# Performance work log

Measured on AMD Instinct MI355X. Metric: run time of the kernel, lower is better.

## Reference

```python
import jax, jax.numpy as jnp
import numpy as np

B, V, L, C = 4, 8, 256, 1024
H, O = 16, 4
Dh = C // H
NEG = -1e9

def setup_inputs() -> dict:
    key = jax.random.key(0)
    ks = jax.random.split(key, 16)
    inp = {}
    inp['v'] = jax.random.normal(ks[0], (B, V, L, C), jnp.float32)
    inp['k'] = jax.random.normal(ks[1], (B, V, L, C), jnp.float32)
    inp['q'] = jax.random.normal(ks[2], (B, V, L, C), jnp.float32)
    inp['masks'] = jax.random.uniform(ks[3], (O, B, V, 1, 1, L)) < 0.15  # True = masked out
    inp['tau'] = jnp.ones((1,), jnp.float32)
    inp['training'] = 1
    u = jax.random.uniform(ks[4], (B, V, O), jnp.float32, minval=1e-20, maxval=1.0)
    inp['gumbel_noise'] = -jnp.log(-jnp.log(u))  # standard Gumbel, = -log(Exp(1))
    s = 1.0 / np.sqrt(C)
    inp['Wv'] = jax.random.normal(ks[5], (C, C), jnp.float32) * s
    inp['bv'] = jnp.zeros((C,), jnp.float32)
    inp['Wk'] = jax.random.normal(ks[6], (C, C), jnp.float32) * s
    inp['bk'] = jnp.zeros((C,), jnp.float32)
    inp['Wq'] = jax.random.normal(ks[7], (C, C), jnp.float32) * s
    inp['bq'] = jnp.zeros((C,), jnp.float32)
    inp['Wm'] = jax.random.normal(ks[8], (C, C), jnp.float32) * s
    inp['bm'] = jnp.zeros((C,), jnp.float32)
    inp['W1'] = jax.random.normal(ks[9], (C, C // 2), jnp.float32) * s
    inp['W2'] = jax.random.normal(ks[10], (C // 2, O), jnp.float32) * (1.0 / np.sqrt(C // 2))
    inp['b2'] = jnp.zeros((O,), jnp.float32)
    return inp


def reference(v, k, q, masks, tau, training, gumbel_noise,
              Wv, bv, Wk, bk, Wq, bq, Wm, bm, W1, W2, b2):
    # --- HardRoutingBlock (pooling='avg'): avg-pool over seq, MLP, gumbel-softmax ---
    pooled = jnp.mean(v, axis=2)                          # [B,V,C]
    h = jax.nn.relu(pooled @ W1)                          # [B,V,C/2]
    logits = h @ W2 + b2                                  # [B,V,O]
    logp = jax.nn.log_softmax(logits, axis=-1)
    alphas = jax.nn.softmax((logp + gumbel_noise) / tau[0], axis=-1)  # [B,V,O]

    # --- multi-head projections: [B,V,L,C] -> [B,V,H,L,Dh] ---
    def split_heads(x):
        return x.reshape(B, V, L, H, Dh).transpose(0, 1, 3, 2, 4)
    vv = split_heads(v @ Wv + bv)
    kk = split_heads(k @ Wk + bk)
    qq = split_heads(q @ Wq + bq)

    scores = jnp.einsum('bvhqd,bvhkd->bvhqk', qq, kk) / np.sqrt(Dh)  # [B,V,H,L,L]
    # per-order masked softmax: masks [O,B,V,1,1,L]
    att = jax.nn.softmax(jnp.where(masks, NEG, scores[None]), axis=-1)  # [O,B,V,H,L,L]
    # routed combination: einsum('bvl,bvlcnm->bvcnm') with l=orders
    att_map = jnp.einsum('bvo,obvhqk->bvhqk', alphas, att)
    atted = jnp.einsum('bvhqk,bvhkd->bvhqd', att_map, vv)  # [B,V,H,L,Dh]
    atted = atted.transpose(0, 1, 3, 2, 4).reshape(B, V, L, C)
    return atted @ Wm + bm
```

## Files before the change

### kernel.cpp

```cpp
#include <hip/hip_runtime.h>

#define B_   4
#define V_   8
#define L_   256
#define C_   1024
#define H_   16
#define O_   4
#define DH_  64
#define BV_  32
#define M_   8192
#define MB_  (1024 * 1024)

typedef short bf16x8 __attribute__((ext_vector_type(8)));
typedef short bf16x4 __attribute__((ext_vector_type(4)));
typedef float f32x4  __attribute__((ext_vector_type(4)));
typedef float f32x16 __attribute__((ext_vector_type(16)));

__device__ __forceinline__ float bflo(unsigned int w) { return __uint_as_float(w << 16); }
__device__ __forceinline__ float bfhi(unsigned int w) { return __uint_as_float(w & 0xffff0000u); }
__device__ __forceinline__ unsigned int f2bfbits(float f) {
    unsigned int i = __float_as_uint(f);
    return (i + 0x7fffu + ((i >> 16) & 1u)) >> 16;
}
__device__ __forceinline__ unsigned int packbf(float a, float b) {
    return f2bfbits(a) | (f2bfbits(b) << 16);
}
__device__ __forceinline__ unsigned int cvtpk_bf16(float lo, float hi) {
    unsigned int r;
    asm("v_cvt_pk_bf16_f32 %0, %1, %2" : "=v"(r) : "v"(lo), "v"(hi));
    return r;
}

typedef const __attribute__((address_space(1))) unsigned int* gas_t;
typedef __attribute__((address_space(3))) unsigned int* las_t;
__device__ __forceinline__ void gll16(const void* g, void* l) {
    __builtin_amdgcn_global_load_lds((gas_t)g, (las_t)l, 16, 0, 0);
}

__device__ __forceinline__ void conv_body(const float* __restrict__ in,
                                          unsigned short* __restrict__ outp,
                                          int blk, int t)
{
    const size_t i = ((size_t)blk * 256 + t) * 8;
    const float4 f0 = *(const float4*)(in + i);
    const float4 f1 = *(const float4*)(in + i + 4);
    uint4 o;
    o.x = packbf(f0.x, f0.y); o.y = packbf(f0.z, f0.w);
    o.z = packbf(f1.x, f1.y); o.w = packbf(f1.z, f1.w);
    *(uint4*)(outp + i) = o;
}

__device__ __forceinline__ void pools_body(const float* __restrict__ v,
                                           float* __restrict__ pbuf2,
                                           int pb, int t)
{
    const int bv = pb >> 3, lc = pb & 7;
    const float* vb = v + (size_t)bv * (L_ * C_) + (size_t)lc * 32 * C_ + t * 4;
    float a0 = 0.f, a1 = 0.f, a2 = 0.f, a3 = 0.f;
#pragma unroll
    for (int l = 0; l < 32; ++l) {
        const float4 f = *(const float4*)(vb + (size_t)l * C_);
        a0 += f.x; a1 += f.y; a2 += f.z; a3 += f.w;
    }
    float4 o; o.x = a0; o.y = a1; o.z = a2; o.w = a3;
    *(float4*)(pbuf2 + ((size_t)lc * 32 + bv) * C_ + t * 4) = o;
}

__device__ __forceinline__ void wprep_body(const float* __restrict__ W,
                                           unsigned short* __restrict__ Wt,
                                           float (*tile)[65], int k0, int n0, int t)
{
    const int r = t >> 2, c4 = (t & 3) * 16;
#pragma unroll
    for (int i = 0; i < 4; ++i) {
        const float4 f = *(const float4*)(W + (size_t)(k0 + r) * C_ + n0 + c4 + i * 4);
        tile[r][c4 + i * 4 + 0] = f.x; tile[r][c4 + i * 4 + 1] = f.y;
        tile[r][c4 + i * 4 + 2] = f.z; tile[r][c4 + i * 4 + 3] = f.w;
    }
    __syncthreads();
    unsigned int ow[8];
#pragma unroll
    for (int p = 0; p < 8; ++p)
        ow[p] = packbf(tile[c4 + 2 * p][r], tile[c4 + 2 * p + 1][r]);
    unsigned short* dst = Wt + (size_t)(n0 + r) * C_ + k0 + c4;
    uint4 o0; o0.x = ow[0]; o0.y = ow[1]; o0.z = ow[2]; o0.w = ow[3];
    uint4 o1; o1.x = ow[4]; o1.y = ow[5]; o1.z = ow[6]; o1.w = ow[7];
    *(uint4*)dst = o0;
    *(uint4*)(dst + 8) = o1;
}

__global__ __launch_bounds__(256) void conv_k(const float* __restrict__ in,
                                              unsigned short* __restrict__ outp)
{ conv_body(in, outp, blockIdx.x, threadIdx.x); }

__global__ __launch_bounds__(256) void pools_k(const float* __restrict__ v,
                                               float* __restrict__ pbuf2)
{ pools_body(v, pbuf2, blockIdx.x, threadIdx.x); }

__global__ __launch_bounds__(256) void wprep_k(const float* __restrict__ W,
                                               unsigned short* __restrict__ Wt)
{
    __shared__ float tile[64][65];
    wprep_body(W, Wt, tile, blockIdx.x * 64, blockIdx.y * 64, threadIdx.x);
}

__global__ __launch_bounds__(1024) void maskpack_k(
    const void* __restrict__ src, unsigned char* __restrict__ dst)
{
    __shared__ int v_word;
    const int t = threadIdx.x;
    if (t == 0) v_word = 1;
    __syncthreads();
    const unsigned int* s32 = (const unsigned int*)src;
    const unsigned int w = s32[t];
    if (w > 1u && w != 0x3F800000u) atomicAnd(&v_word, 0);
    __syncthreads();
    const bool word_mode = (v_word != 0);
    const unsigned char* s8 = (const unsigned char*)src;
#pragma unroll
    for (int i = 0; i < 8; ++i) {
        const int idx = t * 8 + i;
        const int bv = idx >> 8, l = idx & 255;
        unsigned int bits = 0;
#pragma unroll
        for (int o = 0; o < O_; ++o) {
            const int mi = (o * BV_ + bv) * L_ + l;
            const unsigned int m = word_mode ? (s32[mi] != 0u) : (s8[mi] != 0);
            bits |= m << o;
        }
        dst[idx] = (unsigned char)bits;
    }
}

__global__ __launch_bounds__(256) void prep_k(
    const float* __restrict__ q, const float* __restrict__ k, const float* __restrict__ v,
    const void* __restrict__ msk,
    const float* __restrict__ Wq, const float* __restrict__ Wk,
    const float* __restrict__ Wv, const float* __restrict__ Wm,
    unsigned short* __restrict__ cq, unsigned short* __restrict__ ck,
    unsigned short* __restrict__ cv,
    float* __restrict__ pbuf2, unsigned char* __restrict__ mpk,
    unsigned short* __restrict__ Wtb)
{
    __shared__ float tile[64][65];
    const int blk = blockIdx.x;
    const int t = threadIdx.x;
    if (blk < 12288) {
        const int wsel = blk >> 12;
        const float* in = (wsel == 0) ? q : (wsel == 1) ? k : v;
        unsigned short* outp = (wsel == 0) ? cq : (wsel == 1) ? ck : cv;
        conv_body(in, outp, blk & 4095, t);
    } else if (blk < 12544) {
        pools_body(v, pbuf2, blk - 12288, t);
    } else if (blk < 12548) {
        __shared__ int v_word;
        if (t == 0) v_word = 1;
        __syncthreads();
        const unsigned int* s32 = (const unsigned int*)msk;
        const unsigned int w = s32[t];
        if (w > 1u && w != 0x3F800000u) atomicAnd(&v_word, 0);
        __syncthreads();
        const bool word_mode = (v_word != 0);
        const unsigned char* s8 = (const unsigned char*)msk;
        const int tt = (blk - 12544) * 256 + t;
#pragma unroll
        for (int i = 0; i < 8; ++i) {
            const int idx = tt * 8 + i;
            const int bv = idx >> 8, l = idx & 255;
            unsigned int bits = 0;
#pragma unroll
            for (int o = 0; o < O_; ++o) {
                const int mi = (o * BV_ + bv) * L_ + l;
                const unsigned int m = word_mode ? (s32[mi] != 0u) : (s8[mi] != 0);
                bits |= m << o;
            }
            mpk[idx] = (unsigned char)bits;
        }
    } else {
        const int wb = blk - 12548;
        const int wsel = wb >> 8;
        const float* W = (wsel == 0) ? Wq : (wsel == 1) ? Wk : (wsel == 2) ? Wv : Wm;
        unsigned short* Wt = Wtb + (size_t)wsel * (C_ * C_);
        const int b = wb & 255;
        wprep_body(W, Wt, tile, (b & 15) * 64, (b >> 4) * 64, t);
    }
}

__global__ __launch_bounds__(256) void poolr_k(const float* __restrict__ pbuf2,
                                               float* __restrict__ pooled)
{
    const int idx = blockIdx.x * 256 + threadIdx.x;
    float s = 0.f;
#pragma unroll
    for (int p = 0; p < 8; ++p) s += pbuf2[(size_t)p * (32 * C_) + idx];
    pooled[idx] = s * (1.0f / 256.0f);
}

__global__ __launch_bounds__(256) void mlp1_k(const float* __restrict__ pooled,
                                              const float* __restrict__ W1,
                                              float* __restrict__ pbuf)
{
    const int t = threadIdx.x;
    const int col = blockIdx.x * 32 + (t & 31);
    const int b0 = (t >> 5) * 4;
    const int c0 = blockIdx.y * 32;
    float a0 = 0.f, a1 = 0.f, a2 = 0.f, a3 = 0.f;
#pragma unroll
    for (int c = c0; c < c0 + 32; ++c) {
        const float wv = W1[(size_t)c * 512 + col];
        a0 = fmaf(pooled[(size_t)(b0 + 0) * C_ + c], wv, a0);
        a1 = fmaf(pooled[(size_t)(b0 + 1) * C_ + c], wv, a1);
        a2 = fmaf(pooled[(size_t)(b0 + 2) * C_ + c], wv, a2);
        a3 = fmaf(pooled[(size_t)(b0 + 3) * C_ + c], wv, a3);
    }
    const size_t pb = ((size_t)blockIdx.y * 32 + b0) * 512 + col;
    pbuf[pb]        = a0;
    pbuf[pb + 512]  = a1;
    pbuf[pb + 1024] = a2;
    pbuf[pb + 1536] = a3;
}

__global__ __launch_bounds__(256) void mlp2_k(const float* __restrict__ pbuf,
                                              const float* __restrict__ W2,
                                              const float* __restrict__ b2,
                                              const float* __restrict__ gum,
                                              const float* __restrict__ tau,
                                              float* __restrict__ alphas)
{
    __shared__ float red[4][O_];
    const int bv = blockIdx.x, t = threadIdx.x;
    float h0 = 0.f, h1 = 0.f;
#pragma unroll
    for (int ch = 0; ch < 32; ++ch) {
        h0 += pbuf[((size_t)ch * 32 + bv) * 512 + t];
        h1 += pbuf[((size_t)ch * 32 + bv) * 512 + 256 + t];
    }
    h0 = fmaxf(h0, 0.f); h1 = fmaxf(h1, 0.f);
    float part[O_];
#pragma unroll
    for (int o = 0; o < O_; ++o)
        part[o] = h0 * W2[t * O_ + o] + h1 * W2[(t + 256) * O_ + o];
#pragma unroll
    for (int off = 32; off >= 1; off >>= 1) {
#pragma unroll
        for (int o = 0; o < O_; ++o) part[o] += __shfl_down(part[o], off, 64);
    }
    const int wid = t >> 6, lane = t & 63;
    if (lane == 0) {
#pragma unroll
        for (int o = 0; o < O_; ++o) red[wid][o] = part[o];
    }
    __syncthreads();
    if (t == 0) {
        float lg[O_];
#pragma unroll
        for (int o = 0; o < O_; ++o)
            lg[o] = red[0][o] + red[1][o] + red[2][o] + red[3][o] + b2[o];
        float mx = fmaxf(fmaxf(lg[0], lg[1]), fmaxf(lg[2], lg[3]));
        float s = 0.f;
#pragma unroll
        for (int o = 0; o < O_; ++o) s += expf(lg[o] - mx);
        const float lse = logf(s) + mx;
        const float it = 1.0f / tau[0];
        float y[O_];
#pragma unroll
        for (int o = 0; o < O_; ++o) y[o] = (lg[o] - lse + gum[bv * O_ + o]) * it;
        float my = fmaxf(fmaxf(y[0], y[1]), fmaxf(y[2], y[3]));
        float z = 0.f;
#pragma unroll
        for (int o = 0; o < O_; ++o) { y[o] = expf(y[o] - my); z += y[o]; }
        const float iz = 1.0f / z;
#pragma unroll
        for (int o = 0; o < O_; ++o) alphas[bv * O_ + o] = y[o] * iz;
    }
}

template <bool PROJSTORE>
__device__ __forceinline__ void mgemm_body(
    const unsigned short* __restrict__ Ab, const unsigned short* __restrict__ Wt,
    const float* __restrict__ bias, void* __restrict__ out_, int n0, int m0)
{
    __shared__ unsigned short As0[128][64], As1[128][64];
    __shared__ unsigned short Bs0[128][64], Bs1[128][64];
    const int t = threadIdx.x;
    const int w = t >> 6, lane = t & 63;
    const int wm = (w >> 1) * 64, wn = (w & 1) * 64;
    const int fr = lane & 15;
    const int fq = lane >> 4;

    const int sr = w * 8 + (lane >> 3);
    const int sc = ((lane & 7) ^ ((lane >> 3) & 7)) * 8;
    const unsigned short* aP = Ab + (size_t)(m0 + sr) * C_ + sc;
    const unsigned short* bP = Wt + (size_t)(n0 + sr) * C_ + sc;

    const int frm = (fr & 7);

    f32x4 acc[4][4] = {};

#define STAGE(AB, BB, KT)                                                   \
    {                                                                       \
        _Pragma("unroll")                                                   \
        for (int i_ = 0; i_ < 4; ++i_) {                                    \
            gll16(aP + (size_t)i_ * 32 * C_ + (KT), &AB[i_ * 32 + w * 8][0]);\
            gll16(bP + (size_t)i_ * 32 * C_ + (KT), &BB[i_ * 32 + w * 8][0]);\
        }                                                                   \
    }

#define COMPUTE(AB, BB)                                                     \
    {                                                                       \
        _Pragma("unroll")                                                   \
        for (int c_ = 0; c_ < 2; ++c_) {                                    \
            const int rk_ = ((c_ * 4 + fq) ^ frm) * 8;                      \
            bf16x8 af_[4], bf_[4];                                          \
            _Pragma("unroll")                                               \
            for (int i_ = 0; i_ < 4; ++i_)                                  \
                af_[i_] = *(const bf16x8*)&AB[wm + i_ * 16 + fr][rk_];      \
            _Pragma("unroll")                                               \
            for (int j_ = 0; j_ < 4; ++j_)                                  \
                bf_[j_] = *(const bf16x8*)&BB[wn + j_ * 16 + fr][rk_];      \
            _Pragma("unroll")                                               \
            for (int i_ = 0; i_ < 4; ++i_)                                  \
                _Pragma("unroll")                                           \
                for (int j_ = 0; j_ < 4; ++j_)                              \
                    acc[i_][j_] = __builtin_amdgcn_mfma_f32_16x16x32_bf16(  \
                        af_[i_], bf_[j_], acc[i_][j_], 0, 0, 0);            \
        }                                                                   \
    }

    STAGE(As0, Bs0, 0);
#pragma unroll 1
    for (int kt = 0; kt < C_; kt += 128) {
        STAGE(As1, Bs1, kt + 64);
        asm volatile("s_waitcnt vmcnt(8)" ::: "memory");
        __builtin_amdgcn_s_barrier();
        COMPUTE(As0, Bs0);
        __builtin_amdgcn_s_barrier();
        if (kt + 128 < C_) {
            STAGE(As0, Bs0, kt + 128);
            asm volatile("s_waitcnt vmcnt(8)" ::: "memory");
        } else {
            asm volatile("s_waitcnt vmcnt(0)" ::: "memory");
        }
        __builtin_amdgcn_s_barrier();
        COMPUTE(As1, Bs1);
        __builtin_amdgcn_s_barrier();
    }
#undef STAGE
#undef COMPUTE

#pragma unroll
    for (int j = 0; j < 4; ++j) {
        const int gcol = n0 + wn + j * 16 + fr;
        const float bj = bias[gcol];
#pragma unroll
        for (int i = 0; i < 4; ++i) {
#pragma unroll
            for (int r = 0; r < 4; ++r) {
                const int grow = m0 + wm + i * 16 + fq * 4 + r;
                const float val = acc[i][j][r] + bj;
                if (PROJSTORE) {
                    const int bvb = grow >> 8, l = grow & 255;
                    const int hh = gcol >> 6, dh = gcol & 63;
                    ((unsigned short*)out_)[(((size_t)bvb * H_ + hh) * L_ + l) * DH_ + dh] =
                        (unsigned short)f2bfbits(val);
                } else {
                    ((float*)out_)[(size_t)grow * C_ + gcol] = val;
                }
            }
        }
    }
}

template <bool PROJSTORE>
__global__ __launch_bounds__(256) void mgemm_k(
    const unsigned short* __restrict__ Ab, const unsigned short* __restrict__ Wt,
    const float* __restrict__ bias, void* __restrict__ out_)
{
    mgemm_body<PROJSTORE>(Ab, Wt, bias, out_, blockIdx.x * 128, blockIdx.y * 128);
}

__global__ __launch_bounds__(256) void mgemm3_k(
    const unsigned short* __restrict__ cq, const unsigned short* __restrict__ ck,
    const unsigned short* __restrict__ cv, const unsigned short* __restrict__ Wtb,
    const float* __restrict__ bq, const float* __restrict__ bk, const float* __restrict__ bvv,
    unsigned short* __restrict__ qqw, unsigned short* __restrict__ kkw,
    unsigned short* __restrict__ vvw)
{
    const int b = blockIdx.x;
    const int swz = (b & 7) * 192 + (b >> 3);
    const int which = swz >> 9;
    const int g = swz & 511;
    const unsigned short* A = (which == 0) ? cq : (which == 1) ? ck : cv;
    const unsigned short* W = Wtb + (size_t)which * (C_ * C_);
    const float* bias = (which == 0) ? bq : (which == 1) ? bk : bvv;
    unsigned short* outp = (which == 0) ? qqw : (which == 1) ? kkw : vvw;
    mgemm_body<true>(A, W, bias, (void*)outp, (g & 7) * 128, (g >> 3) * 128);
}

__global__ __launch_bounds__(256) void mgemmf_k(
    const unsigned short* __restrict__ Ab, const unsigned short* __restrict__ Wt,
    const float* __restrict__ bias, float* __restrict__ out_)
{
    const int b = blockIdx.x;
    const int swz = (b & 7) * 64 + (b >> 3);
    mgemm_body<false>(Ab, Wt, bias, (void*)out_, (swz & 7) * 128, (swz >> 3) * 128);
}

__global__ __launch_bounds__(256) void attn_k(
    const unsigned short* __restrict__ qq, const unsigned short* __restrict__ kk,
    const unsigned short* __restrict__ vv, const unsigned char* __restrict__ mpk,
    const float* __restrict__ alphas, unsigned short* __restrict__ atted)
{
    __shared__ unsigned short Vt[DH_][260];
    __shared__ unsigned int mkw[64];
    __shared__ float al[O_];
    const int h = blockIdx.x, bv = blockIdx.y;
    const int t = threadIdx.x;
    const int w = t >> 6, lane = t & 63;
    const int fr = lane & 31, hf = lane >> 5;
    const size_t hb = ((size_t)bv * H_ + h) * (L_ * DH_);

    {
        const uint4* gv = (const uint4*)(vv + hb + (size_t)t * DH_);
#pragma unroll
        for (int i = 0; i < 8; ++i) {
            const uint4 wv = gv[i];
            const unsigned int ws4[4] = {wv.x, wv.y, wv.z, wv.w};
#pragma unroll
            for (int jd = 0; jd < 4; ++jd) {
                Vt[i * 8 + jd * 2 + 0][t] = (unsigned short)(ws4[jd] & 0xffffu);
                Vt[i * 8 + jd * 2 + 1][t] = (unsigned short)(ws4[jd] >> 16);
            }
        }
    }
    if (t < 64) mkw[t] = ((const unsigned int*)mpk)[bv * 64 + t];
    if (t < O_) al[t] = alphas[bv * O_ + t];
    __syncthreads();
    const float al0 = al[0], al1 = al[1], al2 = al[2], al3 = al[3];

#pragma unroll 1
    for (int qt = 0; qt < 2; ++qt) {
        const int q32 = w * 64 + qt * 32;
        bf16x8 qf[4];
#pragma unroll
        for (int st = 0; st < 4; ++st)
            qf[st] = *(const bf16x8*)(qq + hb + (size_t)(q32 + fr) * DH_ + st * 16 + hf * 8);

        float T0 = 0.f, T1 = 0.f, T2 = 0.f, T3 = 0.f;
#pragma unroll 1
        for (int j = 0; j < 8; ++j) {
            bf16x8 kf[4];
#pragma unroll
            for (int st = 0; st < 4; ++st)
                kf[st] = *(const bf16x8*)(kk + hb + (size_t)(j * 32 + fr) * DH_ + st * 16 + hf * 8);
            f32x16 s = {};
#pragma unroll
            for (int st = 0; st < 4; ++st)
                s = __builtin_amdgcn_mfma_f32_32x32x16_bf16(kf[st], qf[st], s, 0, 0, 0);
#pragma unroll
            for (int c = 0; c < 4; ++c) {
                const unsigned int iv = (~mkw[j * 8 + c * 2 + hf]) & 0x0F0F0F0Fu;
#pragma unroll
                for (int r = 0; r < 4; ++r) {
                    const float e = __expf(s[c * 4 + r] * 0.125f);
                    const unsigned int nib = iv >> (r * 8);
                    T0 = fmaf(e, (float)( nib       & 1u), T0);
                    T1 = fmaf(e, (float)((nib >> 1) & 1u), T1);
                    T2 = fmaf(e, (float)((nib >> 2) & 1u), T2);
                    T3 = fmaf(e, (float)((nib >> 3) & 1u), T3);
                }
            }
        }
        T0 += __shfl_xor(T0, 32, 64);
        T1 += __shfl_xor(T1, 32, 64);
        T2 += __shfl_xor(T2, 32, 64);
        T3 += __shfl_xor(T3, 32, 64);
        const float c0 = al0 * __builtin_amdgcn_rcpf(fmaxf(T0, 1e-30f));
        const float c1 = al1 * __builtin_amdgcn_rcpf(fmaxf(T1, 1e-30f));
        const float c2 = al2 * __builtin_amdgcn_rcpf(fmaxf(T2, 1e-30f));
        const float c3 = al3 * __builtin_amdgcn_rcpf(fmaxf(T3, 1e-30f));

        f32x16 o0 = {};
        f32x16 o1 = {};
#pragma unroll 1
        for (int j = 0; j < 8; ++j) {
            bf16x8 kf[4];
#pragma unroll
            for (int st = 0; st < 4; ++st)
                kf[st] = *(const bf16x8*)(kk + hb + (size_t)(j * 32 + fr) * DH_ + st * 16 + hf * 8);
            f32x16 s = {};
#pragma unroll
            for (int st = 0; st < 4; ++st)
                s = __builtin_amdgcn_mfma_f32_32x32x16_bf16(kf[st], qf[st], s, 0, 0, 0);

            unsigned int pe[4][2];
#pragma unroll
            for (int c = 0; c < 4; ++c) {
                const unsigned int iv = (~mkw[j * 8 + c * 2 + hf]) & 0x0F0F0F0Fu;
                float p[4];
#pragma unroll
                for (int r = 0; r < 4; ++r) {
                    const float e = __expf(s[c * 4 + r] * 0.125f);
                    const unsigned int nib = iv >> (r * 8);
                    float cf =      c0 * (float)( nib       & 1u);
                    cf = fmaf(c1, (float)((nib >> 1) & 1u), cf);
                    cf = fmaf(c2, (float)((nib >> 2) & 1u), cf);
                    cf = fmaf(c3, (float)((nib >> 3) & 1u), cf);
                    p[r] = e * cf;
                }
                pe[c][0] = cvtpk_bf16(p[0], p[1]);
                pe[c][1] = cvtpk_bf16(p[2], p[3]);
            }
#pragma unroll
            for (int b = 0; b < 2; ++b) {
                const unsigned int qe0 = pe[2 * b][0],     qe1 = pe[2 * b][1];
                const unsigned int qo0 = pe[2 * b + 1][0], qo1 = pe[2 * b + 1][1];
                const unsigned int xe0 = (unsigned int)__shfl_xor((int)qe0, 32, 64);
                const unsigned int xe1 = (unsigned int)__shfl_xor((int)qe1, 32, 64);
                const unsigned int xo0 = (unsigned int)__shfl_xor((int)qo0, 32, 64);
                const unsigned int xo1 = (unsigned int)__shfl_xor((int)qo1, 32, 64);
                union { unsigned int d[4]; bf16x8 v; } pa;
                pa.d[0] = hf ? xo0 : qe0;
                pa.d[1] = hf ? xo1 : qe1;
                pa.d[2] = hf ? qo0 : xe0;
                pa.d[3] = hf ? qo1 : xe1;

                const int kc = j * 32 + b * 16 + hf * 8;
                union { struct { bf16x4 lo, hi; } p2; bf16x8 v; } v0u, v1u;
                v0u.p2.lo = *(const bf16x4*)&Vt[ 0 + fr][kc];
                v0u.p2.hi = *(const bf16x4*)&Vt[ 0 + fr][kc + 4];
                v1u.p2.lo = *(const bf16x4*)&Vt[32 + fr][kc];
                v1u.p2.hi = *(const bf16x4*)&Vt[32 + fr][kc + 4];
                o0 = __builtin_amdgcn_mfma_f32_32x32x16_bf16(pa.v, v0u.v, o0, 0, 0, 0);
                o1 = __builtin_amdgcn_mfma_f32_32x32x16_bf16(pa.v, v1u.v, o1, 0, 0, 0);
            }
        }
#pragma unroll
        for (int reg = 0; reg < 16; ++reg) {
            const int qrow = q32 + (reg & 3) + 8 * (reg >> 2) + 4 * hf;
            unsigned short* dst = atted + ((size_t)bv * L_ + qrow) * C_ + h * DH_;
            dst[fr]      = (unsigned short)f2bfbits(o0[reg]);
            dst[32 + fr] = (unsigned short)f2bfbits(o1[reg]);
        }
    }
}

extern "C" void kernel_launch(void* const* d_in, const int* in_sizes, int n_in,
                              void* d_out, int out_size, void* d_ws, size_t ws_size,
                              hipStream_t stream)
{
    (void)in_sizes; (void)n_in; (void)out_size;
    const float* v   = (const float*)d_in[0];
    const float* k   = (const float*)d_in[1];
    const float* q   = (const float*)d_in[2];
    const void*  msk = d_in[3];
    const float* tau = (const float*)d_in[4];
    const float* gum = (const float*)d_in[6];
    const float* Wv  = (const float*)d_in[7];
    const float* bvp = (const float*)d_in[8];
    const float* Wk  = (const float*)d_in[9];
    const float* bkp = (const float*)d_in[10];
    const float* Wq  = (const float*)d_in[11];
    const float* bqp = (const float*)d_in[12];
    const float* Wm  = (const float*)d_in[13];
    const float* bmp = (const float*)d_in[14];
    const float* W1  = (const float*)d_in[15];
    const float* W2  = (const float*)d_in[16];
    const float* b2  = (const float*)d_in[17];
    float* out = (float*)d_out;

    char* ws = (char*)d_ws;

    if (ws_size >= (size_t)128 * MB_) {
        float* alphas       = (float*)ws;
        unsigned char* mpk  = (unsigned char*)(ws + 1024);
        float* pooled       = (float*)(ws + 16384);
        float* pbuf2        = (float*)(ws + 147456);
        float* pbuf         = (float*)(ws + 1196032);
        unsigned short* Wtb = (unsigned short*)(ws + (size_t)4 * MB_);
        unsigned short* cq  = (unsigned short*)(ws + (size_t)14 * MB_);
        unsigned short* ck  = (unsigned short*)(ws + (size_t)30 * MB_);
        unsigned short* cv  = (unsigned short*)(ws + (size_t)46 * MB_);
        unsigned short* qqw = (unsigned short*)(ws + (size_t)62 * MB_);
        unsigned short* kkw = (unsigned short*)(ws + (size_t)78 * MB_);
        unsigned short* vvw = (unsigned short*)(ws + (size_t)94 * MB_);
        unsigned short* atw = (unsigned short*)(ws + (size_t)110 * MB_);

        hipLaunchKernelGGL(prep_k, dim3(13572), dim3(256), 0, stream,
                           q, k, v, msk, Wq, Wk, Wv, Wm, cq, ck, cv, pbuf2, mpk, Wtb);
        hipLaunchKernelGGL(poolr_k, dim3(128), dim3(256), 0, stream, pbuf2, pooled);
        hipLaunchKernelGGL(mlp1_k, dim3(16, 32), dim3(256), 0, stream, pooled, W1, pbuf);
        hipLaunchKernelGGL(mlp2_k, dim3(BV_), dim3(256), 0, stream,
                           pbuf, W2, b2, gum, tau, alphas);
        hipLaunchKernelGGL(mgemm3_k, dim3(1536), dim3(256), 0, stream,
                           cq, ck, cv, Wtb, bqp, bkp, bvp, qqw, kkw, vvw);
        hipLaunchKernelGGL(attn_k, dim3(H_, BV_), dim3(256), 0, stream,
                           qqw, kkw, vvw, mpk, alphas, atw);
        hipLaunchKernelGGL(mgemmf_k, dim3(512), dim3(256), 0, stream,
                           atw, Wtb + (size_t)3 * (C_ * C_), bmp, out);
    } else {
        float* alphas       = (float*)ws;
        unsigned char* mpk  = (unsigned char*)(ws + 1024);
        float* pooled       = (float*)(ws + 16384);
        float* pbuf2        = (float*)(ws + 147456);
        float* pbuf         = (float*)(ws + 1196032);
        unsigned short* Wt  = (unsigned short*)(ws + 16384);
        unsigned short* qqw = (unsigned short*)(ws + 2113536);
        unsigned short* kkw = qqw + (size_t)M_ * C_;
        unsigned short* vvw = kkw + (size_t)M_ * C_;
        unsigned short* atw = vvw + (size_t)M_ * C_;

        hipLaunchKernelGGL(pools_k, dim3(256), dim3(256), 0, stream, v, pbuf2);
        hipLaunchKernelGGL(poolr_k, dim3(128), dim3(256), 0, stream, pbuf2, pooled);
        hipLaunchKernelGGL(mlp1_k, dim3(16, 32), dim3(256), 0, stream, pooled, W1, pbuf);
        hipLaunchKernelGGL(mlp2_k, dim3(BV_), dim3(256), 0, stream,
                           pbuf, W2, b2, gum, tau, alphas);
        hipLaunchKernelGGL(maskpack_k, dim3(1), dim3(1024), 0, stream, msk, mpk);

        hipLaunchKernelGGL(conv_k, dim3(4096), dim3(256), 0, stream, q, atw);
        hipLaunchKernelGGL(wprep_k, dim3(16, 16), dim3(256), 0, stream, Wq, Wt);
        hipLaunchKernelGGL((mgemm_k<true>), dim3(8, 64), dim3(256), 0, stream,
                           atw, Wt, bqp, (void*)qqw);
        hipLaunchKernelGGL(conv_k, dim3(4096), dim3(256), 0, stream, k, atw);
        hipLaunchKernelGGL(wprep_k, dim3(16, 16), dim3(256), 0, stream, Wk, Wt);
        hipLaunchKernelGGL((mgemm_k<true>), dim3(8, 64), dim3(256), 0, stream,
                           atw, Wt, bkp, (void*)kkw);
        hipLaunchKernelGGL(conv_k, dim3(4096), dim3(256), 0, stream, v, atw);
        hipLaunchKernelGGL(wprep_k, dim3(16, 16), dim3(256), 0, stream, Wv, Wt);
        hipLaunchKernelGGL((mgemm_k<true>), dim3(8, 64), dim3(256), 0, stream,
                           atw, Wt, bvp, (void*)vvw);

        hipLaunchKernelGGL(attn_k, dim3(H_, BV_), dim3(256), 0, stream,
                           qqw, kkw, vvw, mpk, alphas, atw);

        hipLaunchKernelGGL(wprep_k, dim3(16, 16), dim3(256), 0, stream, Wm, Wt);
        hipLaunchKernelGGL((mgemm_k<false>), dim3(8, 64), dim3(256), 0, stream,
                           atw, Wt, bmp, (void*)out);
    }
}
```

Baseline: 183.7 us.

## Fuse pooling reduction, MLP layers and gumbel softmax into one routing kernel

Replaces the three launches poolr_k, mlp1_k and mlp2_k with a single routing_k that runs one block per (b,v). Each block reduces the pooled partials into shared memory, then computes the full 1024-deep first MLP layer per thread before the existing second layer and softmax. This removes two kernel launches and the intermediate pooled/pbuf round trips through global memory. In exchange, the routing work now runs on only 32 blocks with a serial 1024-iteration loop per thread, which reduces parallelism and re-reads W1 once per block.

```diff
diff --git a/kernel.cpp b/kernel.cpp
--- a/kernel.cpp
+++ b/kernel.cpp
@@ -186,56 +186,34 @@
     }
 }
 
-__global__ __launch_bounds__(256) void poolr_k(const float* __restrict__ pbuf2,
-                                               float* __restrict__ pooled)
-{
-    const int idx = blockIdx.x * 256 + threadIdx.x;
-    float s = 0.f;
-#pragma unroll
-    for (int p = 0; p < 8; ++p) s += pbuf2[(size_t)p * (32 * C_) + idx];
-    pooled[idx] = s * (1.0f / 256.0f);
-}
-
-__global__ __launch_bounds__(256) void mlp1_k(const float* __restrict__ pooled,
-                                              const float* __restrict__ W1,
-                                              float* __restrict__ pbuf)
-{
-    const int t = threadIdx.x;
-    const int col = blockIdx.x * 32 + (t & 31);
-    const int b0 = (t >> 5) * 4;
-    const int c0 = blockIdx.y * 32;
-    float a0 = 0.f, a1 = 0.f, a2 = 0.f, a3 = 0.f;
-#pragma unroll
-    for (int c = c0; c < c0 + 32; ++c) {
-        const float wv = W1[(size_t)c * 512 + col];
-        a0 = fmaf(pooled[(size_t)(b0 + 0) * C_ + c], wv, a0);
-        a1 = fmaf(pooled[(size_t)(b0 + 1) * C_ + c], wv, a1);
-        a2 = fmaf(pooled[(size_t)(b0 + 2) * C_ + c], wv, a2);
-        a3 = fmaf(pooled[(size_t)(b0 + 3) * C_ + c], wv, a3);
-    }
-    const size_t pb = ((size_t)blockIdx.y * 32 + b0) * 512 + col;
-    pbuf[pb]        = a0;
-    pbuf[pb + 512]  = a1;
-    pbuf[pb + 1024] = a2;
-    pbuf[pb + 1536] = a3;
-}
-
-__global__ __launch_bounds__(256) void mlp2_k(const float* __restrict__ pbuf,
-                                              const float* __restrict__ W2,
-                                              const float* __restrict__ b2,
-                                              const float* __restrict__ gum,
-                                              const float* __restrict__ tau,
-                                              float* __restrict__ alphas)
-{
+__global__ __launch_bounds__(256) void routing_k(
+    const float* __restrict__ pbuf2, const float* __restrict__ W1,
+    const float* __restrict__ W2, const float* __restrict__ b2,
+    const float* __restrict__ gum, const float* __restrict__ tau,
+    float* __restrict__ alphas)
+{
+    __shared__ float pooled_sh[C_];
     __shared__ float red[4][O_];
     const int bv = blockIdx.x, t = threadIdx.x;
+
+#pragma unroll
+    for (int cc = 0; cc < 4; ++cc) {
+        const int c = cc * 256 + t;
+        float s = 0.f;
+#pragma unroll
+        for (int p = 0; p < 8; ++p) s += pbuf2[((size_t)p * 32 + bv) * C_ + c];
+        pooled_sh[c] = s * (1.0f / 256.0f);
+    }
+    __syncthreads();
+
     float h0 = 0.f, h1 = 0.f;
-#pragma unroll
-    for (int ch = 0; ch < 32; ++ch) {
-        h0 += pbuf[((size_t)ch * 32 + bv) * 512 + t];
-        h1 += pbuf[((size_t)ch * 32 + bv) * 512 + 256 + t];
+    for (int c = 0; c < C_; ++c) {
+        const float p = pooled_sh[c];
+        h0 = fmaf(p, W1[(size_t)c * 512 + t], h0);
+        h1 = fmaf(p, W1[(size_t)c * 512 + 256 + t], h1);
     }
     h0 = fmaxf(h0, 0.f); h1 = fmaxf(h1, 0.f);
+
     float part[O_];
 #pragma unroll
     for (int o = 0; o < O_; ++o)
@@ -574,9 +552,7 @@
     if (ws_size >= (size_t)128 * MB_) {
         float* alphas       = (float*)ws;
         unsigned char* mpk  = (unsigned char*)(ws + 1024);
-        float* pooled       = (float*)(ws + 16384);
         float* pbuf2        = (float*)(ws + 147456);
-        float* pbuf         = (float*)(ws + 1196032);
         unsigned short* Wtb = (unsigned short*)(ws + (size_t)4 * MB_);
         unsigned short* cq  = (unsigned short*)(ws + (size_t)14 * MB_);
         unsigned short* ck  = (unsigned short*)(ws + (size_t)30 * MB_);
@@ -588,10 +564,8 @@
 
         hipLaunchKernelGGL(prep_k, dim3(13572), dim3(256), 0, stream,
                            q, k, v, msk, Wq, Wk, Wv, Wm, cq, ck, cv, pbuf2, mpk, Wtb);
-        hipLaunchKernelGGL(poolr_k, dim3(128), dim3(256), 0, stream, pbuf2, pooled);
-        hipLaunchKernelGGL(mlp1_k, dim3(16, 32), dim3(256), 0, stream, pooled, W1, pbuf);
-        hipLaunchKernelGGL(mlp2_k, dim3(BV_), dim3(256), 0, stream,
-                           pbuf, W2, b2, gum, tau, alphas);
+        hipLaunchKernelGGL(routing_k, dim3(BV_), dim3(256), 0, stream,
+                           pbuf2, W1, W2, b2, gum, tau, alphas);
         hipLaunchKernelGGL(mgemm3_k, dim3(1536), dim3(256), 0, stream,
                            cq, ck, cv, Wtb, bqp, bkp, bvp, qqw, kkw, vvw);
         hipLaunchKernelGGL(attn_k, dim3(H_, BV_), dim3(256), 0, stream,
@@ -601,9 +575,7 @@
     } else {
         float* alphas       = (float*)ws;
         unsigned char* mpk  = (unsigned char*)(ws + 1024);
-        float* pooled       = (float*)(ws + 16384);
         float* pbuf2        = (float*)(ws + 147456);
-        float* pbuf         = (float*)(ws + 1196032);
         unsigned short* Wt  = (unsigned short*)(ws + 16384);
         unsigned short* qqw = (unsigned short*)(ws + 2113536);
         unsigned short* kkw = qqw + (size_t)M_ * C_;
@@ -611,10 +583,8 @@
         unsigned short* atw = vvw + (size_t)M_ * C_;
 
         hipLaunchKernelGGL(pools_k, dim3(256), dim3(256), 0, stream, v, pbuf2);
-        hipLaunchKernelGGL(poolr_k, dim3(128), dim3(256), 0, stream, pbuf2, pooled);
-        hipLaunchKernelGGL(mlp1_k, dim3(16, 32), dim3(256), 0, stream, pooled, W1, pbuf);
-        hipLaunchKernelGGL(mlp2_k, dim3(BV_), dim3(256), 0, stream,
-                           pbuf, W2, b2, gum, tau, alphas);
+        hipLaunchKernelGGL(routing_k, dim3(BV_), dim3(256), 0, stream,
+                           pbuf2, W1, W2, b2, gum, tau, alphas);
         hipLaunchKernelGGL(maskpack_k, dim3(1), dim3(1024), 0, stream, msk, mpk);
 
         hipLaunchKernelGGL(conv_k, dim3(4096), dim3(256), 0, stream, q, atw);
```

After: 222.0 us. 20.8% more time.
